# Optimization experiments

Measured on AMD Instinct MI355X. Metric: run time of the kernel, lower is better.

The kernel has to match this reference:

```python
import jax, jax.numpy as jnp
import numpy as np

FMAP = 56    # feature-map side (seq_len = FMAP**2 = 3136)
WS = 7       # window size
SHIFT = WS // 2  # 3, shifted-window offset
NH = 3       # heads
C = 96       # hidden dim
FF = 384     # feed-forward dim (4*C)
EPS = 1e-5


def _swin_mask():
    # Standard Swin shifted-window attention mask, shape (nW, L, L), values in {0, -1e9}.
    img = np.zeros((FMAP, FMAP), dtype=np.int32)
    slices = (slice(0, -WS), slice(-WS, -SHIFT), slice(-SHIFT, None))
    cnt = 0
    for hs in slices:
        for ws_ in slices:
            img[hs, ws_] = cnt
            cnt += 1
    w = img.reshape(FMAP // WS, WS, FMAP // WS, WS).transpose(0, 2, 1, 3).reshape(-1, WS * WS)
    m = np.where(w[:, None, :] != w[:, :, None], -1e9, 0.0).astype(np.float32)
    return jnp.asarray(m)  # (nW, L, L)


def _ln(x, w, b):
    mu = jnp.mean(x, axis=-1, keepdims=True)
    var = jnp.mean(jnp.square(x - mu), axis=-1, keepdims=True)
    return (x - mu) * jax.lax.rsqrt(var + EPS) * w + b


def setup_inputs() -> dict:
    key = jax.random.key(0)
    ks = jax.random.split(key, 8)
    s = 0.02
    return {
        "x": jax.random.normal(ks[0], (128, FMAP * FMAP, C), dtype=jnp.float32),
        "qkv_w": jax.random.normal(ks[1], (3 * C, C), dtype=jnp.float32) * s,
        "qkv_b": jnp.zeros((3 * C,), dtype=jnp.float32),
        "out_w": jax.random.normal(ks[2], (C, C), dtype=jnp.float32) * s,
        "out_b": jnp.zeros((C,), dtype=jnp.float32),
        "ln1_w": jnp.ones((C,), dtype=jnp.float32),
        "ln1_b": jnp.zeros((C,), dtype=jnp.float32),
        "ln2_w": jnp.ones((C,), dtype=jnp.float32),
        "ln2_b": jnp.zeros((C,), dtype=jnp.float32),
        "ff1_w": jax.random.normal(ks[3], (FF, C), dtype=jnp.float32) * s,
        "ff1_b": jnp.zeros((FF,), dtype=jnp.float32),
        "ff2_w": jax.random.normal(ks[4], (C, FF), dtype=jnp.float32) * s,
        "ff2_b": jnp.zeros((C,), dtype=jnp.float32),
    }


def reference(x, qkv_w, qkv_b, out_w, out_b, ln1_w, ln1_b, ln2_w, ln2_b, ff1_w, ff1_b, ff2_w, ff2_b):
    B, S, Cd = x.shape
    L = WS * WS
    g = FMAP // WS
    nW = g * g
    hd = Cd // NH

    # cyclic shift + window partition: (B, S, C) -> (B*nW, L, C)
    xi = jnp.roll(x.reshape(B, FMAP, FMAP, Cd), (-SHIFT, -SHIFT), axis=(1, 2))
    xw = xi.reshape(B, g, WS, g, WS, Cd).transpose(0, 1, 3, 2, 4, 5).reshape(B * nW, L, Cd)

    mask = _swin_mask()                                  # (nW, L, L)
    mask = jnp.tile(mask, (B, 1, 1))[:, None, :, :]      # (B*nW, 1, L, L)

    # pre-norm MHA
    h = _ln(xw, ln1_w, ln1_b)
    qkv = h @ qkv_w.T + qkv_b
    q, k, v = jnp.split(qkv, 3, axis=-1)
    def heads(t):
        return t.reshape(B * nW, L, NH, hd).transpose(0, 2, 1, 3)  # (B*nW, H, L, hd)
    q, k, v = heads(q), heads(k), heads(v)
    scores = jnp.einsum('bhqd,bhkd->bhqk', q, k) / jnp.sqrt(jnp.float32(hd)) + mask
    attn = jax.nn.softmax(scores, axis=-1)
    o = jnp.einsum('bhqk,bhkd->bhqd', attn, v).transpose(0, 2, 1, 3).reshape(B * nW, L, Cd)
    xw = xw + o @ out_w.T + out_b

    # pre-norm FFN with exact (erf) GELU, as torch activation='gelu'
    h2 = _ln(xw, ln2_w, ln2_b)
    xw = xw + jax.nn.gelu(h2 @ ff1_w.T + ff1_b, approximate=False) @ ff2_w.T + ff2_b

    # window merge + reverse shift
    xo = xw.reshape(B, g, g, WS, WS, Cd).transpose(0, 1, 3, 2, 4, 5).reshape(B, FMAP, FMAP, Cd)
    xo = jnp.roll(xo, (SHIFT, SHIFT), axis=(1, 2))
    return xo.reshape(B, S, Cd)
```

## Files before the change

### kernel.cpp

```cpp
#include <hip/hip_runtime.h>
#include <stdint.h>

#define FMAPD 56
#define WSD 7
#define SHIFTD 3
#define LD 49
#define CD 96
#define NHD 3
#define HDD 32

using u16 = unsigned short;
using u32 = unsigned int;

typedef __attribute__((ext_vector_type(8))) short bh8;
typedef __attribute__((ext_vector_type(4))) float f4;

__device__ __forceinline__ u16 f2b(float f) {
  union { float f; u32 i; } v; v.f = f;
  u32 r = v.i + 0x7fffu + ((v.i >> 16) & 1u);
  return (u16)(r >> 16);
}

#define SH 104
#define SS 200
#define SV 72
#define SP 72

__global__ void cvt_weights(const float* __restrict__ a, const float* __restrict__ b,
                            const float* __restrict__ c, const float* __restrict__ d,
                            u16* __restrict__ ws) {
  int i = blockIdx.x * 256 + threadIdx.x;
  if (i < 27648)       ws[i] = f2b(a[i]);
  else if (i < 36864)  ws[i] = f2b(b[i - 27648]);
  else if (i < 73728)  ws[i] = f2b(c[i - 36864]);
  else if (i < 110592) ws[i] = f2b(d[i - 73728]);
}

__global__ __launch_bounds__(256, 2)
void swin_mfma(const float* __restrict__ gx,
               const float* __restrict__ b_qkv,
               const float* __restrict__ b_out,
               const float* __restrict__ w_ln1, const float* __restrict__ b_ln1,
               const float* __restrict__ w_ln2, const float* __restrict__ b_ln2,
               const float* __restrict__ b_ff1, const float* __restrict__ b_ff2,
               const u16* __restrict__ ws,
               float* __restrict__ gout)
{
  __shared__ __align__(16) u16 s_h [64 * SH];
  __shared__ __align__(16) u16 s_sc[64 * SS];
  __shared__ __align__(16) u16 s_vt[3 * 32 * SV];
  __shared__ __align__(16) u16 s_p [4 * 16 * SP];
  __shared__ int s_id[64];

  const int tid = threadIdx.x;
  const int w = tid >> 6, lane = tid & 63, g = lane >> 4, lq = lane & 15;
  const int blk = blockIdx.x, b = blk >> 6, wr = (blk >> 3) & 7, wc = blk & 7;

  const u16* wsq = ws;
  const u16* wso = ws + 27648;
  const u16* wf1 = ws + 36864;
  const u16* wf2 = ws + 73728;

  if (tid < 64) {
    int id = -1;
    if (tid < 49) {
      int i = tid / 7, j = tid - 7 * i;
      int rp = wr * 7 + i, cp = wc * 7 + j;
      int ri = (rp < 49) ? 0 : ((rp < 53) ? 1 : 2);
      int ci = (cp < 49) ? 0 : ((cp < 53) ? 1 : 2);
      id = ri * 3 + ci;
    }
    s_id[tid] = id;
  }

  float resid[6][4];
  size_t gbase[4];
  bool tval[4];
#pragma unroll
  for (int r = 0; r < 4; ++r) {
    int token = 16 * w + 4 * g + r;
    tval[r] = token < LD;
    int ti = token / 7, tj = token - 7 * ti;
    int row = wr * 7 + ti + SHIFTD; if (row >= FMAPD) row -= FMAPD;
    int col = wc * 7 + tj + SHIFTD; if (col >= FMAPD) col -= FMAPD;
    gbase[r] = ((size_t)b * (FMAPD * FMAPD) + row * FMAPD + col) * (size_t)CD + lq;
#pragma unroll
    for (int t = 0; t < 6; ++t) {
      float v = gx[gbase[r] + 16 * t];
      resid[t][r] = tval[r] ? v : 0.f;
    }
  }

  auto layer_norm = [&](const float* lw, const float* lb) {
    float wv[6], bv[6];
#pragma unroll
    for (int t = 0; t < 6; ++t) { wv[t] = lw[16 * t + lq]; bv[t] = lb[16 * t + lq]; }
#pragma unroll
    for (int r = 0; r < 4; ++r) {
      float s = 0.f, s2 = 0.f;
#pragma unroll
      for (int t = 0; t < 6; ++t) { float v = resid[t][r]; s += v; s2 += v * v; }
#pragma unroll
      for (int m = 1; m <= 8; m <<= 1) { s += __shfl_xor(s, m, 64); s2 += __shfl_xor(s2, m, 64); }
      float mu = s * (1.f / 96.f);
      float rs = rsqrtf(s2 * (1.f / 96.f) - mu * mu + 1e-5f);
      u16* dst = s_h + (16 * w + 4 * g + r) * SH;
#pragma unroll
      for (int t = 0; t < 6; ++t) dst[16 * t + lq] = f2b((resid[t][r] - mu) * rs * wv[t] + bv[t]);
    }
  };
  layer_norm(w_ln1, b_ln1);

  {
    const u16* arow = s_h + (16 * w + lq) * SH;
    bh8 af[3];
#pragma unroll
    for (int kk = 0; kk < 3; ++kk) af[kk] = *(const bh8*)(arow + 32 * kk + 8 * g);
#pragma unroll 3
    for (int t = 0; t < 12; ++t) {
      int n = 16 * t + lq;
      f4 acc = {0.f, 0.f, 0.f, 0.f};
#pragma unroll
      for (int kk = 0; kk < 3; ++kk) {
        bh8 bf = *(const bh8*)(wsq + n * CD + 32 * kk + 8 * g);
        acc = __builtin_amdgcn_mfma_f32_16x16x32_bf16(af[kk], bf, acc, 0, 0, 0);
      }
      float bias = b_qkv[n];
      u16* dst = s_sc + (16 * w + 4 * g) * SS + n;
#pragma unroll
      for (int r = 0; r < 4; ++r) dst[r * SS] = f2b(acc[r] + bias);
    }
#pragma unroll 3
    for (int t = 12; t < 18; ++t) {
      int n = 16 * t + lq;
      f4 acc = {0.f, 0.f, 0.f, 0.f};
#pragma unroll
      for (int kk = 0; kk < 3; ++kk) {
        bh8 bf = *(const bh8*)(wsq + n * CD + 32 * kk + 8 * g);
        acc = __builtin_amdgcn_mfma_f32_16x16x32_bf16(af[kk], bf, acc, 0, 0, 0);
      }
      float bias = b_qkv[n];
      int nn = n - 192;
      u16* dst = s_vt + nn * SV + 16 * w + 4 * g;
#pragma unroll
      for (int r = 0; r < 4; ++r) dst[r] = f2b(acc[r] + bias);
    }
  }
  __syncthreads();

  const float scale = 0.17677669529663687f;
  int rid[4], cid[4];
#pragma unroll
  for (int r = 0; r < 4; ++r) rid[r] = s_id[16 * w + 4 * g + r];
#pragma unroll
  for (int t = 0; t < 4; ++t) cid[t] = s_id[16 * t + lq];

  for (int hh = 0; hh < NHD; ++hh) {
    bh8 qa = *(const bh8*)(s_sc + (16 * w + lq) * SS + hh * 32 + 8 * g);
    f4 sc[4];
#pragma unroll
    for (int t = 0; t < 4; ++t) {
      bh8 kb = *(const bh8*)(s_sc + (16 * t + lq) * SS + CD + hh * 32 + 8 * g);
      f4 z = {0.f, 0.f, 0.f, 0.f};
      sc[t] = __builtin_amdgcn_mfma_f32_16x16x32_bf16(qa, kb, z, 0, 0, 0);
    }
#pragma unroll
    for (int t = 0; t < 4; ++t)
#pragma unroll
      for (int r = 0; r < 4; ++r) {
        float v = sc[t][r] * scale;
        if (rid[r] != cid[t]) v -= 1e9f;
        sc[t][r] = v;
      }
    float pr[4][4];
#pragma unroll
    for (int r = 0; r < 4; ++r) {
      float mx = fmaxf(fmaxf(sc[0][r], sc[1][r]), fmaxf(sc[2][r], sc[3][r]));
#pragma unroll
      for (int m = 1; m <= 8; m <<= 1) mx = fmaxf(mx, __shfl_xor(mx, m, 64));
      float den = 0.f;
#pragma unroll
      for (int t = 0; t < 4; ++t) { float e = __expf(sc[t][r] - mx); pr[t][r] = e; den += e; }
#pragma unroll
      for (int m = 1; m <= 8; m <<= 1) den += __shfl_xor(den, m, 64);
      float inv = 1.0f / den;
#pragma unroll
      for (int t = 0; t < 4; ++t) pr[t][r] *= inv;
    }
    u16* pw = s_p + w * (16 * SP) + (4 * g) * SP;
#pragma unroll
    for (int t = 0; t < 4; ++t)
#pragma unroll
      for (int r = 0; r < 4; ++r) pw[r * SP + 16 * t + lq] = f2b(pr[t][r]);
    const u16* prow = s_p + w * (16 * SP) + lq * SP;
    bh8 pa0 = *(const bh8*)(prow + 8 * g);
    bh8 pa1 = *(const bh8*)(prow + 32 + 8 * g);
#pragma unroll
    for (int nt = 0; nt < 2; ++nt) {
      const u16* vrow = s_vt + (hh * 32 + 16 * nt + lq) * SV;
      bh8 vb0 = *(const bh8*)(vrow + 8 * g);
      bh8 vb1 = *(const bh8*)(vrow + 32 + 8 * g);
      f4 oacc = {0.f, 0.f, 0.f, 0.f};
      oacc = __builtin_amdgcn_mfma_f32_16x16x32_bf16(pa0, vb0, oacc, 0, 0, 0);
      oacc = __builtin_amdgcn_mfma_f32_16x16x32_bf16(pa1, vb1, oacc, 0, 0, 0);
      u16* dst = s_h + (16 * w + 4 * g) * SH + hh * 32 + 16 * nt + lq;
#pragma unroll
      for (int r = 0; r < 4; ++r) dst[r * SH] = f2b(oacc[r]);
    }
  }
  __syncthreads();

  {
    const u16* orow = s_h + (16 * w + lq) * SH;
    bh8 oa[3];
#pragma unroll
    for (int kk = 0; kk < 3; ++kk) oa[kk] = *(const bh8*)(orow + 32 * kk + 8 * g);
#pragma unroll 3
    for (int t = 0; t < 6; ++t) {
      int n = 16 * t + lq;
      f4 acc = {0.f, 0.f, 0.f, 0.f};
#pragma unroll
      for (int kk = 0; kk < 3; ++kk) {
        bh8 bf = *(const bh8*)(wso + n * CD + 32 * kk + 8 * g);
        acc = __builtin_amdgcn_mfma_f32_16x16x32_bf16(oa[kk], bf, acc, 0, 0, 0);
      }
      float bias = b_out[n];
#pragma unroll
      for (int r = 0; r < 4; ++r) resid[t][r] += acc[r] + bias;
    }
  }

  layer_norm(w_ln2, b_ln2);

  {
    const u16* hrow = s_h + (16 * w + lq) * SH;
    bh8 ha[3];
#pragma unroll
    for (int kk = 0; kk < 3; ++kk) ha[kk] = *(const bh8*)(hrow + 32 * kk + 8 * g);
    const u16* frow = s_sc + (16 * w + lq) * SS;
#pragma unroll 1
    for (int half = 0; half < 2; ++half) {
#pragma unroll 3
      for (int t = 0; t < 12; ++t) {
        int n = 192 * half + 16 * t + lq;
        f4 acc = {0.f, 0.f, 0.f, 0.f};
#pragma unroll
        for (int kk = 0; kk < 3; ++kk) {
          bh8 bf = *(const bh8*)(wf1 + n * CD + 32 * kk + 8 * g);
          acc = __builtin_amdgcn_mfma_f32_16x16x32_bf16(ha[kk], bf, acc, 0, 0, 0);
        }
        float bias = b_ff1[n];
        u16* dst = s_sc + (16 * w + 4 * g) * SS + 16 * t + lq;
#pragma unroll
        for (int r = 0; r < 4; ++r) {
          float v = acc[r] + bias;
          float ge = 0.5f * v * (1.0f + erff(v * 0.70710678118654752f));
          dst[r * SS] = f2b(ge);
        }
      }
      bh8 fa[6];
#pragma unroll
      for (int ks = 0; ks < 6; ++ks) fa[ks] = *(const bh8*)(frow + 32 * ks + 8 * g);
#pragma unroll 3
      for (int t = 0; t < 6; ++t) {
        int n = 16 * t + lq;
        f4 acc = {0.f, 0.f, 0.f, 0.f};
#pragma unroll
        for (int ks = 0; ks < 6; ++ks) {
          bh8 bf = *(const bh8*)(wf2 + n * 384 + 192 * half + 32 * ks + 8 * g);
          acc = __builtin_amdgcn_mfma_f32_16x16x32_bf16(fa[ks], bf, acc, 0, 0, 0);
        }
        float bias = half ? 0.f : b_ff2[n];
#pragma unroll
        for (int r = 0; r < 4; ++r) resid[t][r] += acc[r] + bias;
      }
    }
  }

#pragma unroll
  for (int r = 0; r < 4; ++r) {
    if (tval[r]) {
#pragma unroll
      for (int t = 0; t < 6; ++t) gout[gbase[r] + 16 * t] = resid[t][r];
    }
  }
}

extern "C" void kernel_launch(void* const* d_in, const int* in_sizes, int n_in,
                              void* d_out, int out_size, void* d_ws, size_t ws_size,
                              hipStream_t stream) {
  cvt_weights<<<432, 256, 0, stream>>>(
      (const float*)d_in[1], (const float*)d_in[3],
      (const float*)d_in[9], (const float*)d_in[11], (u16*)d_ws);
  swin_mfma<<<8192, 256, 0, stream>>>(
      (const float*)d_in[0],
      (const float*)d_in[2],
      (const float*)d_in[4],
      (const float*)d_in[5], (const float*)d_in[6],
      (const float*)d_in[7], (const float*)d_in[8],
      (const float*)d_in[10], (const float*)d_in[12],
      (const u16*)d_ws, (float*)d_out);
}
```

Baseline: 883.9 us.

## Shrink LDS, transpose MFMA outputs for packed stores, chunk FFN, fast GELU

Reduces shared memory by replacing the wide score buffer with a K buffer reused for FFN chunks and processing the FFN in four 96-wide chunks. This allows three blocks per CU. It swaps MFMA operand order so outputs can be written as packed uint2 bf16 stores, and keeps Q in registers. It also drops one barrier, shortens softmax reductions to two shuffles, hoists bias loads, and replaces erff with an Abramowitz-Stegun polynomial GELU. The polynomial approximation slightly changes numerics, and register pressure under the 3-wave bound may cause spills.

```diff
diff --git a/kernel.cpp b/kernel.cpp
--- a/kernel.cpp
+++ b/kernel.cpp
@@ -2,12 +2,8 @@
 #include <stdint.h>
 
 #define FMAPD 56
-#define WSD 7
-#define SHIFTD 3
 #define LD 49
 #define CD 96
-#define NHD 3
-#define HDD 32
 
 using u16 = unsigned short;
 using u32 = unsigned int;
@@ -20,11 +16,27 @@
   u32 r = v.i + 0x7fffu + ((v.i >> 16) & 1u);
   return (u16)(r >> 16);
 }
+__device__ __forceinline__ u32 pk2(float a, float b) {
+  return (u32)f2b(a) | ((u32)f2b(b) << 16);
+}
+
+__device__ __forceinline__ float gelu_f(float v) {
+  float x = fabsf(v) * 0.70710678118654752f;
+  float t = __builtin_amdgcn_rcpf(fmaf(x, 0.3275911f, 1.0f));
+  float p = fmaf(t, 1.061405429f, -1.453152027f);
+  p = fmaf(p, t, 1.421413741f);
+  p = fmaf(p, t, -0.284496736f);
+  p = fmaf(p, t, 0.254829592f);
+  p = p * t;
+  float e = __expf(-x * x);
+  float q = 0.5f * p * e;
+  float phi = (v >= 0.0f) ? (1.0f - q) : q;
+  return v * phi;
+}
 
 #define SH 104
-#define SS 200
 #define SV 72
-#define SP 72
+#define SP 104
 
 __global__ void cvt_weights(const float* __restrict__ a, const float* __restrict__ b,
                             const float* __restrict__ c, const float* __restrict__ d,
@@ -36,7 +48,7 @@
   else if (i < 110592) ws[i] = f2b(d[i - 73728]);
 }
 
-__global__ __launch_bounds__(256, 2)
+__global__ __launch_bounds__(256, 3)
 void swin_mfma(const float* __restrict__ gx,
                const float* __restrict__ b_qkv,
                const float* __restrict__ b_out,
@@ -47,10 +59,10 @@
                float* __restrict__ gout)
 {
   __shared__ __align__(16) u16 s_h [64 * SH];
-  __shared__ __align__(16) u16 s_sc[64 * SS];
-  __shared__ __align__(16) u16 s_vt[3 * 32 * SV];
+  __shared__ __align__(16) u16 s_k [64 * SH];
+  __shared__ __align__(16) u16 s_vt[96 * SV];
   __shared__ __align__(16) u16 s_p [4 * 16 * SP];
-  __shared__ int s_id[64];
+  __shared__ __align__(16) int s_id[64];
 
   const int tid = threadIdx.x;
   const int w = tid >> 6, lane = tid & 63, g = lane >> 4, lq = lane & 15;
@@ -60,6 +72,8 @@
   const u16* wso = ws + 27648;
   const u16* wf1 = ws + 36864;
   const u16* wf2 = ws + 73728;
+
+  u16* s_pw = s_p + w * (16 * SP);
 
   if (tid < 64) {
     int id = -1;
@@ -81,14 +95,28 @@
     int token = 16 * w + 4 * g + r;
     tval[r] = token < LD;
     int ti = token / 7, tj = token - 7 * ti;
-    int row = wr * 7 + ti + SHIFTD; if (row >= FMAPD) row -= FMAPD;
-    int col = wc * 7 + tj + SHIFTD; if (col >= FMAPD) col -= FMAPD;
+    int row = wr * 7 + ti + 3; if (row >= FMAPD) row -= FMAPD;
+    int col = wc * 7 + tj + 3; if (col >= FMAPD) col -= FMAPD;
     gbase[r] = ((size_t)b * (FMAPD * FMAPD) + row * FMAPD + col) * (size_t)CD + lq;
 #pragma unroll
     for (int t = 0; t < 6; ++t) {
       float v = gx[gbase[r] + 16 * t];
       resid[t][r] = tval[r] ? v : 0.f;
     }
+  }
+
+  float bq[6][4];
+#pragma unroll
+  for (int t = 0; t < 6; ++t) {
+    float4 v = *(const float4*)(b_qkv + 16 * t + 4 * g);
+    bq[t][0] = v.x; bq[t][1] = v.y; bq[t][2] = v.z; bq[t][3] = v.w;
+  }
+  float bvv[6], bov[6], bf2v[6];
+#pragma unroll
+  for (int t = 0; t < 6; ++t) {
+    bvv[t]  = b_qkv[192 + 16 * t + lq];
+    bov[t]  = b_out[16 * t + lq];
+    bf2v[t] = b_ff2[16 * t + lq];
   }
 
   auto layer_norm = [&](const float* lw, const float* lb) {
@@ -116,163 +144,176 @@
     bh8 af[3];
 #pragma unroll
     for (int kk = 0; kk < 3; ++kk) af[kk] = *(const bh8*)(arow + 32 * kk + 8 * g);
-#pragma unroll 3
-    for (int t = 0; t < 12; ++t) {
-      int n = 16 * t + lq;
+
+#pragma unroll
+    for (int t = 0; t < 6; ++t) {
       f4 acc = {0.f, 0.f, 0.f, 0.f};
 #pragma unroll
       for (int kk = 0; kk < 3; ++kk) {
-        bh8 bf = *(const bh8*)(wsq + n * CD + 32 * kk + 8 * g);
+        bh8 bf = *(const bh8*)(wsq + (16 * t + lq) * CD + 32 * kk + 8 * g);
+        acc = __builtin_amdgcn_mfma_f32_16x16x32_bf16(bf, af[kk], acc, 0, 0, 0);
+      }
+      uint2 u; u.x = pk2(acc[0] + bq[t][0], acc[1] + bq[t][1]);
+      u.y = pk2(acc[2] + bq[t][2], acc[3] + bq[t][3]);
+      *(uint2*)(s_pw + lq * SP + 16 * t + 4 * g) = u;
+    }
+#pragma unroll
+    for (int t = 0; t < 6; ++t) {
+      f4 acc = {0.f, 0.f, 0.f, 0.f};
+#pragma unroll
+      for (int kk = 0; kk < 3; ++kk) {
+        bh8 bf = *(const bh8*)(wsq + (96 + 16 * t + lq) * CD + 32 * kk + 8 * g);
+        acc = __builtin_amdgcn_mfma_f32_16x16x32_bf16(bf, af[kk], acc, 0, 0, 0);
+      }
+      uint2 u; u.x = pk2(acc[0], acc[1]); u.y = pk2(acc[2], acc[3]);
+      *(uint2*)(s_k + (16 * w + lq) * SH + 16 * t + 4 * g) = u;
+    }
+#pragma unroll
+    for (int t = 0; t < 6; ++t) {
+      f4 acc = {0.f, 0.f, 0.f, 0.f};
+#pragma unroll
+      for (int kk = 0; kk < 3; ++kk) {
+        bh8 bf = *(const bh8*)(wsq + (192 + 16 * t + lq) * CD + 32 * kk + 8 * g);
         acc = __builtin_amdgcn_mfma_f32_16x16x32_bf16(af[kk], bf, acc, 0, 0, 0);
       }
-      float bias = b_qkv[n];
-      u16* dst = s_sc + (16 * w + 4 * g) * SS + n;
-#pragma unroll
-      for (int r = 0; r < 4; ++r) dst[r * SS] = f2b(acc[r] + bias);
-    }
-#pragma unroll 3
-    for (int t = 12; t < 18; ++t) {
-      int n = 16 * t + lq;
-      f4 acc = {0.f, 0.f, 0.f, 0.f};
-#pragma unroll
-      for (int kk = 0; kk < 3; ++kk) {
-        bh8 bf = *(const bh8*)(wsq + n * CD + 32 * kk + 8 * g);
-        acc = __builtin_amdgcn_mfma_f32_16x16x32_bf16(af[kk], bf, acc, 0, 0, 0);
-      }
-      float bias = b_qkv[n];
-      int nn = n - 192;
-      u16* dst = s_vt + nn * SV + 16 * w + 4 * g;
-#pragma unroll
-      for (int r = 0; r < 4; ++r) dst[r] = f2b(acc[r] + bias);
-    }
-  }
+      float bias = bvv[t];
+      uint2 u; u.x = pk2(acc[0] + bias, acc[1] + bias);
+      u.y = pk2(acc[2] + bias, acc[3] + bias);
+      *(uint2*)(s_vt + (16 * t + lq) * SV + 16 * w + 4 * g) = u;
+    }
+  }
+  bh8 qa[3];
+#pragma unroll
+  for (int hh = 0; hh < 3; ++hh) qa[hh] = *(const bh8*)(s_pw + lq * SP + 32 * hh + 8 * g);
+
   __syncthreads();
 
+  const int id_i = s_id[16 * w + lq];
+  int idj[4][4];
+#pragma unroll
+  for (int t = 0; t < 4; ++t) {
+    int4 v = *(const int4*)(s_id + 16 * t + 4 * g);
+    idj[t][0] = v.x; idj[t][1] = v.y; idj[t][2] = v.z; idj[t][3] = v.w;
+  }
   const float scale = 0.17677669529663687f;
-  int rid[4], cid[4];
-#pragma unroll
-  for (int r = 0; r < 4; ++r) rid[r] = s_id[16 * w + 4 * g + r];
-#pragma unroll
-  for (int t = 0; t < 4; ++t) cid[t] = s_id[16 * t + lq];
-
-  for (int hh = 0; hh < NHD; ++hh) {
-    bh8 qa = *(const bh8*)(s_sc + (16 * w + lq) * SS + hh * 32 + 8 * g);
+
+#pragma unroll
+  for (int hh = 0; hh < 3; ++hh) {
     f4 sc[4];
 #pragma unroll
     for (int t = 0; t < 4; ++t) {
-      bh8 kb = *(const bh8*)(s_sc + (16 * t + lq) * SS + CD + hh * 32 + 8 * g);
+      bh8 kb = *(const bh8*)(s_k + (16 * t + lq) * SH + 32 * hh + 8 * g);
       f4 z = {0.f, 0.f, 0.f, 0.f};
-      sc[t] = __builtin_amdgcn_mfma_f32_16x16x32_bf16(qa, kb, z, 0, 0, 0);
-    }
+      sc[t] = __builtin_amdgcn_mfma_f32_16x16x32_bf16(kb, qa[hh], z, 0, 0, 0);
+    }
+    float pv[4][4];
+    float mx = -3.0e38f;
 #pragma unroll
     for (int t = 0; t < 4; ++t)
 #pragma unroll
       for (int r = 0; r < 4; ++r) {
         float v = sc[t][r] * scale;
-        if (rid[r] != cid[t]) v -= 1e9f;
-        sc[t][r] = v;
-      }
-    float pr[4][4];
-#pragma unroll
-    for (int r = 0; r < 4; ++r) {
-      float mx = fmaxf(fmaxf(sc[0][r], sc[1][r]), fmaxf(sc[2][r], sc[3][r]));
-#pragma unroll
-      for (int m = 1; m <= 8; m <<= 1) mx = fmaxf(mx, __shfl_xor(mx, m, 64));
-      float den = 0.f;
-#pragma unroll
-      for (int t = 0; t < 4; ++t) { float e = __expf(sc[t][r] - mx); pr[t][r] = e; den += e; }
-#pragma unroll
-      for (int m = 1; m <= 8; m <<= 1) den += __shfl_xor(den, m, 64);
-      float inv = 1.0f / den;
-#pragma unroll
-      for (int t = 0; t < 4; ++t) pr[t][r] *= inv;
-    }
-    u16* pw = s_p + w * (16 * SP) + (4 * g) * SP;
+        v = (id_i != idj[t][r]) ? v - 1e9f : v;
+        pv[t][r] = v;
+        mx = fmaxf(mx, v);
+      }
+    mx = fmaxf(mx, __shfl_xor(mx, 16, 64));
+    mx = fmaxf(mx, __shfl_xor(mx, 32, 64));
+    float den = 0.f;
 #pragma unroll
     for (int t = 0; t < 4; ++t)
 #pragma unroll
-      for (int r = 0; r < 4; ++r) pw[r * SP + 16 * t + lq] = f2b(pr[t][r]);
-    const u16* prow = s_p + w * (16 * SP) + lq * SP;
-    bh8 pa0 = *(const bh8*)(prow + 8 * g);
-    bh8 pa1 = *(const bh8*)(prow + 32 + 8 * g);
+      for (int r = 0; r < 4; ++r) { float e = __expf(pv[t][r] - mx); pv[t][r] = e; den += e; }
+    den += __shfl_xor(den, 16, 64);
+    den += __shfl_xor(den, 32, 64);
+    float inv = 1.0f / den;
+#pragma unroll
+    for (int t = 0; t < 4; ++t) {
+      uint2 u; u.x = pk2(pv[t][0] * inv, pv[t][1] * inv);
+      u.y = pk2(pv[t][2] * inv, pv[t][3] * inv);
+      *(uint2*)(s_pw + lq * SP + 16 * t + 4 * g) = u;
+    }
+    bh8 pa0 = *(const bh8*)(s_pw + lq * SP + 8 * g);
+    bh8 pa1 = *(const bh8*)(s_pw + lq * SP + 32 + 8 * g);
 #pragma unroll
     for (int nt = 0; nt < 2; ++nt) {
-      const u16* vrow = s_vt + (hh * 32 + 16 * nt + lq) * SV;
+      const u16* vrow = s_vt + (32 * hh + 16 * nt + lq) * SV;
       bh8 vb0 = *(const bh8*)(vrow + 8 * g);
       bh8 vb1 = *(const bh8*)(vrow + 32 + 8 * g);
-      f4 oacc = {0.f, 0.f, 0.f, 0.f};
-      oacc = __builtin_amdgcn_mfma_f32_16x16x32_bf16(pa0, vb0, oacc, 0, 0, 0);
-      oacc = __builtin_amdgcn_mfma_f32_16x16x32_bf16(pa1, vb1, oacc, 0, 0, 0);
-      u16* dst = s_h + (16 * w + 4 * g) * SH + hh * 32 + 16 * nt + lq;
-#pragma unroll
-      for (int r = 0; r < 4; ++r) dst[r * SH] = f2b(oacc[r]);
-    }
-  }
-  __syncthreads();
+      f4 o = {0.f, 0.f, 0.f, 0.f};
+      o = __builtin_amdgcn_mfma_f32_16x16x32_bf16(vb0, pa0, o, 0, 0, 0);
+      o = __builtin_amdgcn_mfma_f32_16x16x32_bf16(vb1, pa1, o, 0, 0, 0);
+      uint2 u; u.x = pk2(o[0], o[1]); u.y = pk2(o[2], o[3]);
+      *(uint2*)(s_h + (16 * w + lq) * SH + 32 * hh + 16 * nt + 4 * g) = u;
+    }
+  }
 
   {
     const u16* orow = s_h + (16 * w + lq) * SH;
     bh8 oa[3];
 #pragma unroll
     for (int kk = 0; kk < 3; ++kk) oa[kk] = *(const bh8*)(orow + 32 * kk + 8 * g);
-#pragma unroll 3
-    for (int t = 0; t < 6; ++t) {
-      int n = 16 * t + lq;
+#pragma unroll
+    for (int t = 0; t < 6; ++t) {
       f4 acc = {0.f, 0.f, 0.f, 0.f};
 #pragma unroll
       for (int kk = 0; kk < 3; ++kk) {
-        bh8 bf = *(const bh8*)(wso + n * CD + 32 * kk + 8 * g);
+        bh8 bf = *(const bh8*)(wso + (16 * t + lq) * CD + 32 * kk + 8 * g);
         acc = __builtin_amdgcn_mfma_f32_16x16x32_bf16(oa[kk], bf, acc, 0, 0, 0);
       }
-      float bias = b_out[n];
-#pragma unroll
-      for (int r = 0; r < 4; ++r) resid[t][r] += acc[r] + bias;
+#pragma unroll
+      for (int r = 0; r < 4; ++r) resid[t][r] += acc[r] + bov[t];
     }
   }
 
   layer_norm(w_ln2, b_ln2);
+#pragma unroll
+  for (int t = 0; t < 6; ++t)
+#pragma unroll
+    for (int r = 0; r < 4; ++r) resid[t][r] += bf2v[t];
+
+  __syncthreads();
 
   {
     const u16* hrow = s_h + (16 * w + lq) * SH;
     bh8 ha[3];
 #pragma unroll
     for (int kk = 0; kk < 3; ++kk) ha[kk] = *(const bh8*)(hrow + 32 * kk + 8 * g);
-    const u16* frow = s_sc + (16 * w + lq) * SS;
+    const u16* frow = s_k + (16 * w + lq) * SH;
 #pragma unroll 1
-    for (int half = 0; half < 2; ++half) {
-#pragma unroll 3
-      for (int t = 0; t < 12; ++t) {
-        int n = 192 * half + 16 * t + lq;
+    for (int qq = 0; qq < 4; ++qq) {
+      float bq1[6][4];
+#pragma unroll
+      for (int t = 0; t < 6; ++t) {
+        float4 v = *(const float4*)(b_ff1 + 96 * qq + 16 * t + 4 * g);
+        bq1[t][0] = v.x; bq1[t][1] = v.y; bq1[t][2] = v.z; bq1[t][3] = v.w;
+      }
+#pragma unroll
+      for (int t = 0; t < 6; ++t) {
         f4 acc = {0.f, 0.f, 0.f, 0.f};
 #pragma unroll
         for (int kk = 0; kk < 3; ++kk) {
-          bh8 bf = *(const bh8*)(wf1 + n * CD + 32 * kk + 8 * g);
-          acc = __builtin_amdgcn_mfma_f32_16x16x32_bf16(ha[kk], bf, acc, 0, 0, 0);
+          bh8 bf = *(const bh8*)(wf1 + (96 * qq + 16 * t + lq) * CD + 32 * kk + 8 * g);
+          acc = __builtin_amdgcn_mfma_f32_16x16x32_bf16(bf, ha[kk], acc, 0, 0, 0);
         }
-        float bias = b_ff1[n];
-        u16* dst = s_sc + (16 * w + 4 * g) * SS + 16 * t + lq;
-#pragma unroll
-        for (int r = 0; r < 4; ++r) {
-          float v = acc[r] + bias;
-          float ge = 0.5f * v * (1.0f + erff(v * 0.70710678118654752f));
-          dst[r * SS] = f2b(ge);
-        }
-      }
-      bh8 fa[6];
-#pragma unroll
-      for (int ks = 0; ks < 6; ++ks) fa[ks] = *(const bh8*)(frow + 32 * ks + 8 * g);
-#pragma unroll 3
+        uint2 u;
+        u.x = pk2(gelu_f(acc[0] + bq1[t][0]), gelu_f(acc[1] + bq1[t][1]));
+        u.y = pk2(gelu_f(acc[2] + bq1[t][2]), gelu_f(acc[3] + bq1[t][3]));
+        *(uint2*)(s_k + (16 * w + lq) * SH + 16 * t + 4 * g) = u;
+      }
+      bh8 fa[3];
+#pragma unroll
+      for (int ks = 0; ks < 3; ++ks) fa[ks] = *(const bh8*)(frow + 32 * ks + 8 * g);
+#pragma unroll
       for (int t = 0; t < 6; ++t) {
-        int n = 16 * t + lq;
         f4 acc = {0.f, 0.f, 0.f, 0.f};
 #pragma unroll
-        for (int ks = 0; ks < 6; ++ks) {
-          bh8 bf = *(const bh8*)(wf2 + n * 384 + 192 * half + 32 * ks + 8 * g);
+        for (int ks = 0; ks < 3; ++ks) {
+          bh8 bf = *(const bh8*)(wf2 + (16 * t + lq) * 384 + 96 * qq + 32 * ks + 8 * g);
           acc = __builtin_amdgcn_mfma_f32_16x16x32_bf16(fa[ks], bf, acc, 0, 0, 0);
         }
-        float bias = half ? 0.f : b_ff2[n];
-#pragma unroll
-        for (int r = 0; r < 4; ++r) resid[t][r] += acc[r] + bias;
+#pragma unroll
+        for (int r = 0; r < 4; ++r) resid[t][r] += acc[r];
       }
     }
   }
```

After: 876.8 us. Within noise of the previous version (-0.8%).
